# Optimization experiments

Hardware: AMD Instinct MI355X
Metric: run time of the kernel (lower is better)

The kernel has to match this reference:

```python
import jax, jax.numpy as jnp
import numpy as np

N_NODES = 50000
N_EDGES = 800000
IN_F, HID, OUT, FC_OUT = 192, 128, 64, 192


def setup_inputs() -> dict:
    key = jax.random.key(0)
    ks = jax.random.split(key, 12)
    s = 0.05
    return {
        "x": jax.random.normal(ks[0], (N_NODES, IN_F), dtype=jnp.float32),
        "edge_index": jax.random.randint(ks[1], (2, N_EDGES), 0, N_NODES, dtype=jnp.int64),
        "W1": jax.random.normal(ks[2], (IN_F, HID), dtype=jnp.float32) * s,
        "b1": jnp.zeros((HID,), jnp.float32),
        "Wg": jax.random.normal(ks[3], (HID, HID), dtype=jnp.float32) * s,
        "a_src": jax.random.normal(ks[4], (HID,), dtype=jnp.float32) * s,
        "a_dst": jax.random.normal(ks[5], (HID,), dtype=jnp.float32) * s,
        "bg": jnp.zeros((HID,), jnp.float32),
        "W2": jax.random.normal(ks[6], (HID, OUT), dtype=jnp.float32) * s,
        "b2": jnp.zeros((OUT,), jnp.float32),
        "Wf": jax.random.normal(ks[7], (OUT, FC_OUT), dtype=jnp.float32) * s,
        "bf": jnp.zeros((FC_OUT,), jnp.float32),
    }


def reference(x, edge_index, W1, b1, Wg, a_src, a_dst, bg, W2, b2, Wf, bf):
    N = x.shape[0]
    loops = jnp.arange(N, dtype=edge_index.dtype)
    src = jnp.concatenate([edge_index[0], loops])  # [E+N]
    dst = jnp.concatenate([edge_index[1], loops])

    # GCN symmetric normalization with self-loops (PyG gcn_norm)
    deg = jax.ops.segment_sum(jnp.ones_like(dst, dtype=x.dtype), dst, num_segments=N)
    dinv = jax.lax.rsqrt(jnp.maximum(deg, 1.0))  # deg >= 1 due to self-loops
    norm = dinv[src] * dinv[dst]  # [E+N]

    def gcn(h, W, b):
        h = h @ W
        out = jax.ops.segment_sum(h[src] * norm[:, None], dst, num_segments=N)
        return out + b

    h = gcn(x, W1, b1)  # [N, HID]

    # GAT layer (1 head, PyG defaults: self-loops, LeakyReLU(0.2), softmax over dst)
    hg = h @ Wg
    al = hg @ a_src  # [N]
    ar = hg @ a_dst  # [N]
    e = jax.nn.leaky_relu(al[src] + ar[dst], 0.2)  # [E+N]
    emax = jax.ops.segment_max(e, dst, num_segments=N)
    ex = jnp.exp(e - emax[dst])
    denom = jax.ops.segment_sum(ex, dst, num_segments=N)
    alpha = ex / denom[dst]
    h = jax.ops.segment_sum(hg[src] * alpha[:, None], dst, num_segments=N) + bg

    h = jax.nn.relu(h)
    h = gcn(h, W2, b2)  # [N, OUT]
    return h @ Wf + bf  # [N, 192]
```

## Files before the change

### kernel.cpp

```cpp
#include <hip/hip_runtime.h>
#include <hip/hip_fp16.h>
#include <cstdint>
#include <cstddef>

#define NN 50000
#define NE 800000
#define RNG 8
#define RSZ ((NN + RNG - 1) / RNG)
#define FIL_CPR 256
#define FILB (RNG*FIL_CPR)
#define CAP 64

typedef _Float16 half8 __attribute__((ext_vector_type(8)));
typedef float    f32x4 __attribute__((ext_vector_type(4)));

static __device__ __forceinline__ float lrelu02(float x){ return x > 0.f ? x : 0.2f*x; }

static __device__ __forceinline__ float2 h2f(uint32_t u){
  __half2 h = *reinterpret_cast<__half2*>(&u);
  return __half22float2(h);
}
static __device__ __forceinline__ uint32_t f2h(float a, float b){
  __half2 h = __floats2half2_rn(a, b);
  return *reinterpret_cast<uint32_t*>(&h);
}
static __device__ __forceinline__ void acc8p(float* acc, uint4 raw, float p){
  float2 f0=h2f(raw.x), f1=h2f(raw.y), f2=h2f(raw.z), f3=h2f(raw.w);
  acc[0]+=p*f0.x; acc[1]+=p*f0.y; acc[2]+=p*f1.x; acc[3]+=p*f1.y;
  acc[4]+=p*f2.x; acc[5]+=p*f2.y; acc[6]+=p*f3.x; acc[7]+=p*f3.y;
}
static __device__ __forceinline__ void acc8s(float* acc, uint4 raw){
  float2 f0=h2f(raw.x), f1=h2f(raw.y), f2=h2f(raw.z), f3=h2f(raw.w);
  acc[0]+=f0.x; acc[1]+=f0.y; acc[2]+=f1.x; acc[3]+=f1.y;
  acc[4]+=f2.x; acc[5]+=f2.y; acc[6]+=f3.x; acc[7]+=f3.y;
}

__global__ __launch_bounds__(256) void pack_all_kernel(
    const float* __restrict__ W1, const float* __restrict__ Wg,
    const float* __restrict__ W2, const float* __restrict__ Wf,
    _Float16* __restrict__ B1, _Float16* __restrict__ B2,
    _Float16* __restrict__ B3, _Float16* __restrict__ B4,
    int* __restrict__ fillp)
{
  const int b = blockIdx.x;
  if (b >= 240){
    const int i = (b - 240)*256 + threadIdx.x;
    if (i < NN) fillp[i] = 0;
    return;
  }
  const float* B; _Float16* O; int K, N, base;
  if      (b < 96)  { B = W1; O = B1; K = 192; N = 128; base = 0;   }
  else if (b < 160) { B = Wg; O = B2; K = 128; N = 128; base = 96;  }
  else if (b < 192) { B = W2; O = B3; K = 128; N = 64;  base = 160; }
  else              { B = Wf; O = B4; K = 64;  N = 192; base = 192; }
  const int i = (b - base)*256 + threadIdx.x;
  if (i >= K*N) return;
  const int j    = i & 7;
  const int lane = (i >> 3) & 63;
  const int tile = i >> 9;
  const int ntl  = N >> 4;
  const int ct   = tile % ntl;
  const int k0   = (tile / ntl) << 5;
  const int k = k0 + ((lane >> 4) << 3) + j;
  const int n = (ct << 4) + (lane & 15);
  O[i] = (_Float16)B[(size_t)k*N + n];
}

template<int K, int NT, bool AHALF, bool HALF_OUT, bool DOTS>
static __device__ __forceinline__ void gemm_block(
    const void* __restrict__ Av, const _Float16* __restrict__ Bsw,
    const float* __restrict__ bias, const float* __restrict__ rowscale,
    const float* __restrict__ avs, const float* __restrict__ avd,
    float* __restrict__ al, float* __restrict__ ar,
    void* __restrict__ Cv, int M, int N, int bm, int t)
{
  constexpr int NTL = NT*4;
  const int w    = t >> 6;
  const int lane = t & 63;
  const int m    = lane & 15;
  const int quad = lane >> 4;

  f32x4 acc[NTL];
  #pragma unroll
  for (int ct = 0; ct < NTL; ++ct) acc[ct] = (f32x4){0.f,0.f,0.f,0.f};

  const int row = bm + w*16 + m;
  const _Float16* bp = Bsw + lane*8;

  #pragma unroll
  for (int k0 = 0; k0 < K; k0 += 32){
    union { half8 h; uint4 u; uint32_t w[4]; } ua;
    if constexpr (AHALF){
      if (row < M){
        ua.u = *(const uint4*)((const _Float16*)Av + (size_t)row*K + k0 + quad*8);
      } else {
        ua.u = make_uint4(0u,0u,0u,0u);
      }
    } else {
      if (row < M){
        const float* Arow = (const float*)Av + (size_t)row*K;
        const float4 va = *(const float4*)(Arow + k0 + quad*8);
        const float4 vb = *(const float4*)(Arow + k0 + quad*8 + 4);
        ua.w[0] = f2h(va.x, va.y);
        ua.w[1] = f2h(va.z, va.w);
        ua.w[2] = f2h(vb.x, vb.y);
        ua.w[3] = f2h(vb.z, vb.w);
      } else {
        ua.u = make_uint4(0u,0u,0u,0u);
      }
    }
    const half8 af = ua.h;
    #pragma unroll
    for (int ct = 0; ct < NTL; ++ct){
      const half8 bf = *(const half8*)(bp + ((size_t)((k0>>5)*NTL + ct))*512);
      acc[ct] = __builtin_amdgcn_mfma_f32_16x16x32_f16(af, bf, acc[ct], 0, 0, 0);
    }
  }

  float rs[4];
  #pragma unroll
  for (int reg = 0; reg < 4; ++reg){
    const int r = bm + w*16 + quad*4 + reg;
    rs[reg] = (rowscale && r < M) ? rowscale[r] : 1.f;
  }
  float dal[4] = {0.f,0.f,0.f,0.f};
  float dar[4] = {0.f,0.f,0.f,0.f};
  #pragma unroll
  for (int ct = 0; ct < NTL; ++ct){
    const int colg = ct*16 + m;
    const float bv = bias ? bias[colg] : 0.f;
    float s_c = 0.f, d_c = 0.f;
    if constexpr (DOTS){ s_c = avs[colg]; d_c = avd[colg]; }
    #pragma unroll
    for (int reg = 0; reg < 4; ++reg){
      const int r = bm + w*16 + quad*4 + reg;
      if (r < M){
        const float v = rs[reg]*acc[ct][reg] + bv;
        if constexpr (DOTS){ dal[reg] += v*s_c; dar[reg] += v*d_c; }
        if constexpr (HALF_OUT){
          ((__half*)Cv)[(size_t)r*N + colg] = __float2half(v);
        } else {
          ((float*)Cv)[(size_t)r*N + colg] = v;
        }
      }
    }
  }
  if constexpr (DOTS){
    #pragma unroll
    for (int off = 1; off < 16; off <<= 1){
      #pragma unroll
      for (int reg = 0; reg < 4; ++reg){
        dal[reg] += __shfl_xor(dal[reg], off, 64);
        dar[reg] += __shfl_xor(dar[reg], off, 64);
      }
    }
    if (m == 0){
      #pragma unroll
      for (int reg = 0; reg < 4; ++reg){
        const int r = bm + w*16 + quad*4 + reg;
        if (r < M){
          al[r] = dal[reg];
          ar[r] = dar[reg];
        }
      }
    }
  }
}

template<int K, int NT, bool AHALF, bool HALF_OUT, bool DOTS>
__global__ __launch_bounds__(256) void gemm_mfma_kernel(
    const void* __restrict__ Av, const _Float16* __restrict__ Bsw,
    const float* __restrict__ bias, const float* __restrict__ rowscale,
    const float* __restrict__ avs, const float* __restrict__ avd,
    float* __restrict__ al, float* __restrict__ ar,
    void* __restrict__ Cv, int M, int N)
{
  gemm_block<K,NT,AHALF,HALF_OUT,DOTS>(Av, Bsw, bias, rowscale, avs, avd, al, ar,
                                       Cv, M, N, blockIdx.x*64, threadIdx.x);
}

__global__ __launch_bounds__(256) void gemm1_fill_kernel(
    const float* __restrict__ A, const _Float16* __restrict__ B1,
    __half* __restrict__ C, int M, int gm,
    const int* __restrict__ src, const int* __restrict__ dst,
    int* __restrict__ fillp, int* __restrict__ col, int E)
{
  if (blockIdx.x < (unsigned)gm){
    gemm_block<192,2,false,true,false>(A, B1, nullptr, nullptr, nullptr, nullptr,
                                       nullptr, nullptr, C, M, 128,
                                       blockIdx.x*64, threadIdx.x);
    return;
  }
  const int fb = blockIdx.x - gm;
  const int r  = fb % RNG;
  const int i  = fb / RNG;
  const int lo = r * RSZ;
  const int hi = min(lo + RSZ, NN);
  const int cs = (E + FIL_CPR - 1) / FIL_CPR;
  const int e1 = min((i+1)*cs, E);
  int e = i*cs + threadIdx.x;
  for (; e + 768 < e1; e += 1024){
    const int d0 = dst[e];       const int d1 = dst[e+256];
    const int d2 = dst[e+512];   const int d3 = dst[e+768];
    const int s0 = src[e];       const int s1 = src[e+256];
    const int s2 = src[e+512];   const int s3 = src[e+768];
    if (d0 >= lo && d0 < hi){ col[(d0<<6) + atomicAdd(&fillp[d0],1)] = s0; }
    if (d1 >= lo && d1 < hi){ col[(d1<<6) + atomicAdd(&fillp[d1],1)] = s1; }
    if (d2 >= lo && d2 < hi){ col[(d2<<6) + atomicAdd(&fillp[d2],1)] = s2; }
    if (d3 >= lo && d3 < hi){ col[(d3<<6) + atomicAdd(&fillp[d3],1)] = s3; }
  }
  for (; e < e1; e += 256){
    const int d = dst[e];
    if (d >= lo && d < hi){ col[(d<<6) + atomicAdd(&fillp[d],1)] = src[e]; }
  }
}

__global__ __launch_bounds__(256) void dinv_kernel(const int* __restrict__ len,
      float* __restrict__ dinv, int N){
  const int i = blockIdx.x*256 + threadIdx.x;
  if (i < N) dinv[i] = rsqrtf((float)(len[i] + 1));
}

__global__ __launch_bounds__(256) void gcn_agg128d_kernel(
    const __half* __restrict__ H, const int* __restrict__ len, const int* __restrict__ col,
    const float* __restrict__ dinv, const float* __restrict__ bias,
    __half* __restrict__ out, int N)
{
  const int t  = threadIdx.x;
  const int n  = blockIdx.x * 16 + (t >> 4);
  const int gl = t & 15;
  if (n >= N) return;
  const float dn = dinv[n];
  float acc[8];
  {
    uint4 raw = *(const uint4*)(H + (size_t)n*128 + gl*8);
    float2 f0=h2f(raw.x), f1=h2f(raw.y), f2=h2f(raw.z), f3=h2f(raw.w);
    acc[0]=dn*f0.x; acc[1]=dn*f0.y; acc[2]=dn*f1.x; acc[3]=dn*f1.y;
    acc[4]=dn*f2.x; acc[5]=dn*f2.y; acc[6]=dn*f3.x; acc[7]=dn*f3.y;
  }
  const int s0 = n << 6;
  const int s1 = s0 + len[n];
  for (int c0 = s0; c0 < s1; c0 += 16){
    const int nc = min(16, s1 - c0);
    int   sl = (gl < nc) ? col[c0 + gl] : 0;
    float dl = (gl < nc) ? dinv[sl] : 0.f;
    #pragma unroll 2
    for (int j = 0; j < nc; ++j){
      const int   s = __shfl(sl, j, 16);
      const float p = __shfl(dl, j, 16);
      acc8p(acc, *(const uint4*)(H + (size_t)s*128 + gl*8), p);
    }
  }
  const float* bp = bias + gl*8;
  float4 b0 = *(const float4*)(bp);
  float4 b1 = *(const float4*)(bp + 4);
  uint4 o;
  o.x = f2h(dn*acc[0] + b0.x, dn*acc[1] + b0.y);
  o.y = f2h(dn*acc[2] + b0.z, dn*acc[3] + b0.w);
  o.z = f2h(dn*acc[4] + b1.x, dn*acc[5] + b1.y);
  o.w = f2h(dn*acc[6] + b1.z, dn*acc[7] + b1.w);
  *(uint4*)(out + (size_t)n*128 + gl*8) = o;
}

__global__ __launch_bounds__(256) void gcn_agg64_kernel(
    const __half* __restrict__ H, const int* __restrict__ len, const int* __restrict__ col,
    const float* __restrict__ dinv, const float* __restrict__ bias,
    __half* __restrict__ out, int N)
{
  const int t  = threadIdx.x;
  const int n  = blockIdx.x * 32 + (t >> 3);
  const int gl = t & 7;
  if (n >= N) return;
  const float dn = dinv[n];
  float acc[8];
  {
    uint4 raw = *(const uint4*)(H + (size_t)n*64 + gl*8);
    float2 f0=h2f(raw.x), f1=h2f(raw.y), f2=h2f(raw.z), f3=h2f(raw.w);
    acc[0]=f0.x; acc[1]=f0.y; acc[2]=f1.x; acc[3]=f1.y;
    acc[4]=f2.x; acc[5]=f2.y; acc[6]=f3.x; acc[7]=f3.y;
  }
  const int s0 = n << 6;
  const int s1 = s0 + len[n];
  for (int c0 = s0; c0 < s1; c0 += 8){
    const int nc = min(8, s1 - c0);
    int sl = (gl < nc) ? col[c0 + gl] : 0;
    #pragma unroll 2
    for (int j = 0; j < nc; ++j){
      const int s = __shfl(sl, j, 8);
      acc8s(acc, *(const uint4*)(H + (size_t)s*64 + gl*8));
    }
  }
  const float* bp = bias + gl*8;
  float4 b0 = *(const float4*)(bp);
  float4 b1 = *(const float4*)(bp + 4);
  uint4 o;
  o.x = f2h(dn*acc[0] + b0.x, dn*acc[1] + b0.y);
  o.y = f2h(dn*acc[2] + b0.z, dn*acc[3] + b0.w);
  o.z = f2h(dn*acc[4] + b1.x, dn*acc[5] + b1.y);
  o.w = f2h(dn*acc[6] + b1.z, dn*acc[7] + b1.w);
  *(uint4*)(out + (size_t)n*64 + gl*8) = o;
}

__global__ __launch_bounds__(256) void gat_agg_kernel(
    const __half* __restrict__ HG, const int* __restrict__ len, const int* __restrict__ col,
    const float* __restrict__ al, const float* __restrict__ ar,
    const float* __restrict__ bias, __half* __restrict__ out, int N)
{
  const int t  = threadIdx.x;
  const int n  = blockIdx.x * 16 + (t >> 4);
  const int gl = t & 15;
  if (n >= N) return;
  const float arn = ar[n];
  const float pself = __expf(lrelu02(al[n] + arn));
  float lpart = 0.f;
  float acc[8];
  {
    uint4 raw = *(const uint4*)(HG + (size_t)n*128 + gl*8);
    float2 f0=h2f(raw.x), f1=h2f(raw.y), f2=h2f(raw.z), f3=h2f(raw.w);
    acc[0]=pself*f0.x; acc[1]=pself*f0.y; acc[2]=pself*f1.x; acc[3]=pself*f1.y;
    acc[4]=pself*f2.x; acc[5]=pself*f2.y; acc[6]=pself*f3.x; acc[7]=pself*f3.y;
  }
  const int s0 = n << 6;
  const int s1 = s0 + len[n];
  for (int c0 = s0; c0 < s1; c0 += 16){
    const int nc = min(16, s1 - c0);
    int   sl = (gl < nc) ? col[c0 + gl] : 0;
    float pl = (gl < nc) ? __expf(lrelu02(al[sl] + arn)) : 0.f;
    lpart += pl;
    #pragma unroll 2
    for (int j = 0; j < nc; ++j){
      const int   s = __shfl(sl, j, 16);
      const float p = __shfl(pl, j, 16);
      acc8p(acc, *(const uint4*)(HG + (size_t)s*128 + gl*8), p);
    }
  }
  #pragma unroll
  for (int off = 8; off > 0; off >>= 1) lpart += __shfl_xor(lpart, off, 16);
  const float inv = 1.f / (pself + lpart);
  const float* bp = bias + gl*8;
  float4 b0 = *(const float4*)(bp);
  float4 b1 = *(const float4*)(bp + 4);
  uint4 o;
  o.x = f2h(fmaxf(acc[0]*inv + b0.x, 0.f), fmaxf(acc[1]*inv + b0.y, 0.f));
  o.y = f2h(fmaxf(acc[2]*inv + b0.z, 0.f), fmaxf(acc[3]*inv + b0.w, 0.f));
  o.z = f2h(fmaxf(acc[4]*inv + b1.x, 0.f), fmaxf(acc[5]*inv + b1.y, 0.f));
  o.w = f2h(fmaxf(acc[6]*inv + b1.z, 0.f), fmaxf(acc[7]*inv + b1.w, 0.f));
  *(uint4*)(out + (size_t)n*128 + gl*8) = o;
}

extern "C" void kernel_launch(void* const* d_in, const int* in_sizes, int n_in,
                              void* d_out, int out_size, void* d_ws, size_t ws_size,
                              hipStream_t stream)
{
  const float* x     = (const float*)d_in[0];
  const int*   ei    = (const int*)d_in[1];
  const float* W1    = (const float*)d_in[2];
  const float* b1    = (const float*)d_in[3];
  const float* Wg    = (const float*)d_in[4];
  const float* a_src = (const float*)d_in[5];
  const float* a_dst = (const float*)d_in[6];
  const float* bg    = (const float*)d_in[7];
  const float* W2    = (const float*)d_in[8];
  const float* b2    = (const float*)d_in[9];
  const float* Wf    = (const float*)d_in[10];
  const float* bf    = (const float*)d_in[11];
  const int N = NN, E = NE;
  const int* src = ei;
  const int* dst = ei + E;

  char* p = (char*)d_ws;
  auto alloc = [&](size_t bytes)->char*{
    char* r = p; p += (bytes + 511) & ~size_t(511); return r;
  };
  int*      fillp = (int*)     alloc((size_t)N*4);
  int*      col   = (int*)     alloc((size_t)N*CAP*4);
  float*    dinv  = (float*)   alloc((size_t)N*4);
  float*    alar_ = (float*)   alloc((size_t)N*8);
  __half*   H16   = (__half*)  alloc((size_t)N*128*2);
  __half*   Hb    = (__half*)  alloc((size_t)N*128*2);
  _Float16* B1    = (_Float16*)alloc(24576*2);
  _Float16* B2    = (_Float16*)alloc(16384*2);
  _Float16* B3    = (_Float16*)alloc(8192*2);
  _Float16* B4    = (_Float16*)alloc(12288*2);
  float*    al    = alar_;
  float*    ar    = alar_ + N;

  const int gm  = (N + 63) / 64;
  const int g16 = (N + 15) / 16;
  const int g32 = (N + 31) / 32;

  pack_all_kernel<<<240 + (NN + 255)/256, 256, 0, stream>>>(
      W1, Wg, W2, Wf, B1, B2, B3, B4, fillp);

  gemm1_fill_kernel<<<gm + FILB, 256, 0, stream>>>(
      x, B1, H16, N, gm, src, dst, fillp, col, E);

  dinv_kernel<<<(N + 255)/256, 256, 0, stream>>>(fillp, dinv, N);

  gcn_agg128d_kernel<<<g16, 256, 0, stream>>>(H16, fillp, col, dinv, b1, Hb, N);
  gemm_mfma_kernel<128,2,true,true,true><<<gm, 256, 0, stream>>>(
      Hb, B2, nullptr, nullptr, a_src, a_dst, al, ar, H16, N, 128);
  gat_agg_kernel<<<g16, 256, 0, stream>>>(H16, fillp, col, al, ar, bg, Hb, N);
  gemm_mfma_kernel<128,1,true,true,false><<<gm, 256, 0, stream>>>(
      Hb, B3, nullptr, dinv, nullptr, nullptr, nullptr, nullptr, H16, N, 64);
  gcn_agg64_kernel<<<g32, 256, 0, stream>>>(H16, fillp, col, dinv, b2, Hb, N);
  gemm_mfma_kernel<64,3,true,false,false><<<gm, 256, 0, stream>>>(
      Hb, B4, bf, nullptr, nullptr, nullptr, nullptr, nullptr, d_out, N, 192);
}
```

Before: 276.7 us.

## Fold Wg into W1 by associativity and fuse attention dots into first aggregation

```diff
diff --git a/kernel.cpp b/kernel.cpp
--- a/kernel.cpp
+++ b/kernel.cpp
@@ -38,21 +38,30 @@
 __global__ __launch_bounds__(256) void pack_all_kernel(
     const float* __restrict__ W1, const float* __restrict__ Wg,
     const float* __restrict__ W2, const float* __restrict__ Wf,
-    _Float16* __restrict__ B1, _Float16* __restrict__ B2,
-    _Float16* __restrict__ B3, _Float16* __restrict__ B4,
-    int* __restrict__ fillp)
+    const float* __restrict__ b1,
+    _Float16* __restrict__ B1, _Float16* __restrict__ B3, _Float16* __restrict__ B4,
+    float* __restrict__ bg1, int* __restrict__ fillp)
 {
   const int b = blockIdx.x;
-  if (b >= 240){
-    const int i = (b - 240)*256 + threadIdx.x;
-    if (i < NN) fillp[i] = 0;
+  if (b >= 176){
+    if (b < 372){
+      const int i = (b - 176)*256 + threadIdx.x;
+      if (i < NN) fillp[i] = 0;
+    } else {
+      const int n = threadIdx.x;
+      if (n < 128){
+        float s = 0.f;
+        #pragma unroll 4
+        for (int c = 0; c < 128; ++c) s += b1[c]*Wg[c*128 + n];
+        bg1[n] = s;
+      }
+    }
     return;
   }
-  const float* B; _Float16* O; int K, N, base;
-  if      (b < 96)  { B = W1; O = B1; K = 192; N = 128; base = 0;   }
-  else if (b < 160) { B = Wg; O = B2; K = 128; N = 128; base = 96;  }
-  else if (b < 192) { B = W2; O = B3; K = 128; N = 64;  base = 160; }
-  else              { B = Wf; O = B4; K = 64;  N = 192; base = 192; }
+  const float* B; _Float16* O; int K, N, base; bool fused = false;
+  if      (b < 96)  { B = W1; O = B1; K = 192; N = 128; base = 0;  fused = true; }
+  else if (b < 128) { B = W2; O = B3; K = 128; N = 64;  base = 96;  }
+  else              { B = Wf; O = B4; K = 64;  N = 192; base = 128; }
   const int i = (b - base)*256 + threadIdx.x;
   if (i >= K*N) return;
   const int j    = i & 7;
@@ -63,15 +72,20 @@
   const int k0   = (tile / ntl) << 5;
   const int k = k0 + ((lane >> 4) << 3) + j;
   const int n = (ct << 4) + (lane & 15);
-  O[i] = (_Float16)B[(size_t)k*N + n];
-}
-
-template<int K, int NT, bool AHALF, bool HALF_OUT, bool DOTS>
+  if (fused){
+    float s = 0.f;
+    #pragma unroll 4
+    for (int c = 0; c < 128; ++c) s += W1[k*128 + c]*Wg[c*128 + n];
+    O[i] = (_Float16)s;
+  } else {
+    O[i] = (_Float16)B[(size_t)k*N + n];
+  }
+}
+
+template<int K, int NT, bool AHALF, bool HALF_OUT, bool RSLEN>
 static __device__ __forceinline__ void gemm_block(
     const void* __restrict__ Av, const _Float16* __restrict__ Bsw,
-    const float* __restrict__ bias, const float* __restrict__ rowscale,
-    const float* __restrict__ avs, const float* __restrict__ avd,
-    float* __restrict__ al, float* __restrict__ ar,
+    const float* __restrict__ bias, const int* __restrict__ rslen,
     void* __restrict__ Cv, int M, int N, int bm, int t)
 {
   constexpr int NTL = NT*4;
@@ -121,22 +135,18 @@
   #pragma unroll
   for (int reg = 0; reg < 4; ++reg){
     const int r = bm + w*16 + quad*4 + reg;
-    rs[reg] = (rowscale && r < M) ? rowscale[r] : 1.f;
-  }
-  float dal[4] = {0.f,0.f,0.f,0.f};
-  float dar[4] = {0.f,0.f,0.f,0.f};
+    rs[reg] = 1.f;
+    if constexpr (RSLEN){ if (r < M) rs[reg] = rsqrtf((float)(rslen[r] + 1)); }
+  }
   #pragma unroll
   for (int ct = 0; ct < NTL; ++ct){
     const int colg = ct*16 + m;
     const float bv = bias ? bias[colg] : 0.f;
-    float s_c = 0.f, d_c = 0.f;
-    if constexpr (DOTS){ s_c = avs[colg]; d_c = avd[colg]; }
     #pragma unroll
     for (int reg = 0; reg < 4; ++reg){
       const int r = bm + w*16 + quad*4 + reg;
       if (r < M){
         const float v = rs[reg]*acc[ct][reg] + bv;
-        if constexpr (DOTS){ dal[reg] += v*s_c; dar[reg] += v*d_c; }
         if constexpr (HALF_OUT){
           ((__half*)Cv)[(size_t)r*N + colg] = __float2half(v);
         } else {
@@ -145,38 +155,16 @@
       }
     }
   }
-  if constexpr (DOTS){
-    #pragma unroll
-    for (int off = 1; off < 16; off <<= 1){
-      #pragma unroll
-      for (int reg = 0; reg < 4; ++reg){
-        dal[reg] += __shfl_xor(dal[reg], off, 64);
-        dar[reg] += __shfl_xor(dar[reg], off, 64);
-      }
-    }
-    if (m == 0){
-      #pragma unroll
-      for (int reg = 0; reg < 4; ++reg){
-        const int r = bm + w*16 + quad*4 + reg;
-        if (r < M){
-          al[r] = dal[reg];
-          ar[r] = dar[reg];
-        }
-      }
-    }
-  }
-}
-
-template<int K, int NT, bool AHALF, bool HALF_OUT, bool DOTS>
+}
+
+template<int K, int NT, bool AHALF, bool HALF_OUT, bool RSLEN>
 __global__ __launch_bounds__(256) void gemm_mfma_kernel(
     const void* __restrict__ Av, const _Float16* __restrict__ Bsw,
-    const float* __restrict__ bias, const float* __restrict__ rowscale,
-    const float* __restrict__ avs, const float* __restrict__ avd,
-    float* __restrict__ al, float* __restrict__ ar,
+    const float* __restrict__ bias, const int* __restrict__ rslen,
     void* __restrict__ Cv, int M, int N)
 {
-  gemm_block<K,NT,AHALF,HALF_OUT,DOTS>(Av, Bsw, bias, rowscale, avs, avd, al, ar,
-                                       Cv, M, N, blockIdx.x*64, threadIdx.x);
+  gemm_block<K,NT,AHALF,HALF_OUT,RSLEN>(Av, Bsw, bias, rslen, Cv, M, N,
+                                        blockIdx.x*64, threadIdx.x);
 }
 
 __global__ __launch_bounds__(256) void gemm1_fill_kernel(
@@ -186,8 +174,7 @@
     int* __restrict__ fillp, int* __restrict__ col, int E)
 {
   if (blockIdx.x < (unsigned)gm){
-    gemm_block<192,2,false,true,false>(A, B1, nullptr, nullptr, nullptr, nullptr,
-                                       nullptr, nullptr, C, M, 128,
+    gemm_block<192,2,false,true,false>(A, B1, nullptr, nullptr, C, M, 128,
                                        blockIdx.x*64, threadIdx.x);
     return;
   }
@@ -215,90 +202,57 @@
   }
 }
 
-__global__ __launch_bounds__(256) void dinv_kernel(const int* __restrict__ len,
-      float* __restrict__ dinv, int N){
-  const int i = blockIdx.x*256 + threadIdx.x;
-  if (i < N) dinv[i] = rsqrtf((float)(len[i] + 1));
-}
-
-__global__ __launch_bounds__(256) void gcn_agg128d_kernel(
-    const __half* __restrict__ H, const int* __restrict__ len, const int* __restrict__ col,
-    const float* __restrict__ dinv, const float* __restrict__ bias,
-    __half* __restrict__ out, int N)
+__global__ __launch_bounds__(256) void agg1_kernel(
+    const __half* __restrict__ T, const int* __restrict__ len, const int* __restrict__ col,
+    const float* __restrict__ bg1, const float* __restrict__ avs,
+    const float* __restrict__ avd,
+    __half* __restrict__ hg, float* __restrict__ al, float* __restrict__ ar, int N)
 {
   const int t  = threadIdx.x;
   const int n  = blockIdx.x * 16 + (t >> 4);
   const int gl = t & 15;
   if (n >= N) return;
-  const float dn = dinv[n];
+  const int ln = len[n];
+  const float dn = rsqrtf((float)(ln + 1));
   float acc[8];
   {
-    uint4 raw = *(const uint4*)(H + (size_t)n*128 + gl*8);
+    uint4 raw = *(const uint4*)(T + (size_t)n*128 + gl*8);
     float2 f0=h2f(raw.x), f1=h2f(raw.y), f2=h2f(raw.z), f3=h2f(raw.w);
     acc[0]=dn*f0.x; acc[1]=dn*f0.y; acc[2]=dn*f1.x; acc[3]=dn*f1.y;
     acc[4]=dn*f2.x; acc[5]=dn*f2.y; acc[6]=dn*f3.x; acc[7]=dn*f3.y;
   }
   const int s0 = n << 6;
-  const int s1 = s0 + len[n];
+  const int s1 = s0 + ln;
   for (int c0 = s0; c0 < s1; c0 += 16){
     const int nc = min(16, s1 - c0);
     int   sl = (gl < nc) ? col[c0 + gl] : 0;
-    float dl = (gl < nc) ? dinv[sl] : 0.f;
-    #pragma unroll 2
+    float dl = (gl < nc) ? rsqrtf((float)(len[sl] + 1)) : 0.f;
+    #pragma unroll 4
     for (int j = 0; j < nc; ++j){
       const int   s = __shfl(sl, j, 16);
       const float p = __shfl(dl, j, 16);
-      acc8p(acc, *(const uint4*)(H + (size_t)s*128 + gl*8), p);
-    }
-  }
-  const float* bp = bias + gl*8;
-  float4 b0 = *(const float4*)(bp);
-  float4 b1 = *(const float4*)(bp + 4);
+      acc8p(acc, *(const uint4*)(T + (size_t)s*128 + gl*8), p);
+    }
+  }
+  const float* bp = bg1 + gl*8;
+  float v[8];
+  #pragma unroll
+  for (int i = 0; i < 8; ++i) v[i] = dn*acc[i] + bp[i];
   uint4 o;
-  o.x = f2h(dn*acc[0] + b0.x, dn*acc[1] + b0.y);
-  o.y = f2h(dn*acc[2] + b0.z, dn*acc[3] + b0.w);
-  o.z = f2h(dn*acc[4] + b1.x, dn*acc[5] + b1.y);
-  o.w = f2h(dn*acc[6] + b1.z, dn*acc[7] + b1.w);
-  *(uint4*)(out + (size_t)n*128 + gl*8) = o;
-}
-
-__global__ __launch_bounds__(256) void gcn_agg64_kernel(
-    const __half* __restrict__ H, const int* __restrict__ len, const int* __restrict__ col,
-    const float* __restrict__ dinv, const float* __restrict__ bias,
-    __half* __restrict__ out, int N)
-{
-  const int t  = threadIdx.x;
-  const int n  = blockIdx.x * 32 + (t >> 3);
-  const int gl = t & 7;
-  if (n >= N) return;
-  const float dn = dinv[n];
-  float acc[8];
-  {
-    uint4 raw = *(const uint4*)(H + (size_t)n*64 + gl*8);
-    float2 f0=h2f(raw.x), f1=h2f(raw.y), f2=h2f(raw.z), f3=h2f(raw.w);
-    acc[0]=f0.x; acc[1]=f0.y; acc[2]=f1.x; acc[3]=f1.y;
-    acc[4]=f2.x; acc[5]=f2.y; acc[6]=f3.x; acc[7]=f3.y;
-  }
-  const int s0 = n << 6;
-  const int s1 = s0 + len[n];
-  for (int c0 = s0; c0 < s1; c0 += 8){
-    const int nc = min(8, s1 - c0);
-    int sl = (gl < nc) ? col[c0 + gl] : 0;
-    #pragma unroll 2
-    for (int j = 0; j < nc; ++j){
-      const int s = __shfl(sl, j, 8);
-      acc8s(acc, *(const uint4*)(H + (size_t)s*64 + gl*8));
-    }
-  }
-  const float* bp = bias + gl*8;
-  float4 b0 = *(const float4*)(bp);
-  float4 b1 = *(const float4*)(bp + 4);
-  uint4 o;
-  o.x = f2h(dn*acc[0] + b0.x, dn*acc[1] + b0.y);
-  o.y = f2h(dn*acc[2] + b0.z, dn*acc[3] + b0.w);
-  o.z = f2h(dn*acc[4] + b1.x, dn*acc[5] + b1.y);
-  o.w = f2h(dn*acc[6] + b1.z, dn*acc[7] + b1.w);
-  *(uint4*)(out + (size_t)n*64 + gl*8) = o;
+  o.x = f2h(v[0], v[1]); o.y = f2h(v[2], v[3]);
+  o.z = f2h(v[4], v[5]); o.w = f2h(v[6], v[7]);
+  *(uint4*)(hg + (size_t)n*128 + gl*8) = o;
+  const float* asp = avs + gl*8;
+  const float* adp = avd + gl*8;
+  float sal = 0.f, sar = 0.f;
+  #pragma unroll
+  for (int i = 0; i < 8; ++i){ sal += v[i]*asp[i]; sar += v[i]*adp[i]; }
+  #pragma unroll
+  for (int off = 8; off > 0; off >>= 1){
+    sal += __shfl_xor(sal, off, 16);
+    sar += __shfl_xor(sar, off, 16);
+  }
+  if (gl == 0){ al[n] = sal; ar[n] = sar; }
 }
 
 __global__ __launch_bounds__(256) void gat_agg_kernel(
@@ -327,7 +281,7 @@
     int   sl = (gl < nc) ? col[c0 + gl] : 0;
     float pl = (gl < nc) ? __expf(lrelu02(al[sl] + arn)) : 0.f;
     lpart += pl;
-    #pragma unroll 2
+    #pragma unroll 4
     for (int j = 0; j < nc; ++j){
       const int   s = __shfl(sl, j, 16);
       const float p = __shfl(pl, j, 16);
@@ -346,6 +300,45 @@
   o.z = f2h(fmaxf(acc[4]*inv + b1.x, 0.f), fmaxf(acc[5]*inv + b1.y, 0.f));
   o.w = f2h(fmaxf(acc[6]*inv + b1.z, 0.f), fmaxf(acc[7]*inv + b1.w, 0.f));
   *(uint4*)(out + (size_t)n*128 + gl*8) = o;
+}
+
+__global__ __launch_bounds__(256) void gcn_agg64_kernel(
+    const __half* __restrict__ H, const int* __restrict__ len, const int* __restrict__ col,
+    const float* __restrict__ bias, __half* __restrict__ out, int N)
+{
+  const int t  = threadIdx.x;
+  const int n  = blockIdx.x * 32 + (t >> 3);
+  const int gl = t & 7;
+  if (n >= N) return;
+  const int ln = len[n];
+  const float dn = rsqrtf((float)(ln + 1));
+  float acc[8];
+  {
+    uint4 raw = *(const uint4*)(H + (size_t)n*64 + gl*8);
+    float2 f0=h2f(raw.x), f1=h2f(raw.y), f2=h2f(raw.z), f3=h2f(raw.w);
+    acc[0]=f0.x; acc[1]=f0.y; acc[2]=f1.x; acc[3]=f1.y;
+    acc[4]=f2.x; acc[5]=f2.y; acc[6]=f3.x; acc[7]=f3.y;
+  }
+  const int s0 = n << 6;
+  const int s1 = s0 + ln;
+  for (int c0 = s0; c0 < s1; c0 += 8){
+    const int nc = min(8, s1 - c0);
+    int sl = (gl < nc) ? col[c0 + gl] : 0;
+    #pragma unroll 4
+    for (int j = 0; j < nc; ++j){
+      const int s = __shfl(sl, j, 8);
+      acc8s(acc, *(const uint4*)(H + (size_t)s*64 + gl*8));
+    }
+  }
+  const float* bp = bias + gl*8;
+  float4 b0 = *(const float4*)(bp);
+  float4 b1 = *(const float4*)(bp + 4);
+  uint4 o;
+  o.x = f2h(dn*acc[0] + b0.x, dn*acc[1] + b0.y);
+  o.y = f2h(dn*acc[2] + b0.z, dn*acc[3] + b0.w);
+  o.z = f2h(dn*acc[4] + b1.x, dn*acc[5] + b1.y);
+  o.w = f2h(dn*acc[6] + b1.z, dn*acc[7] + b1.w);
+  *(uint4*)(out + (size_t)n*64 + gl*8) = o;
 }
 
 extern "C" void kernel_launch(void* const* d_in, const int* in_sizes, int n_in,
@@ -374,14 +367,13 @@
   };
   int*      fillp = (int*)     alloc((size_t)N*4);
   int*      col   = (int*)     alloc((size_t)N*CAP*4);
-  float*    dinv  = (float*)   alloc((size_t)N*4);
   float*    alar_ = (float*)   alloc((size_t)N*8);
-  __half*   H16   = (__half*)  alloc((size_t)N*128*2);
-  __half*   Hb    = (__half*)  alloc((size_t)N*128*2);
+  __half*   HA    = (__half*)  alloc((size_t)N*128*2);
+  __half*   HB    = (__half*)  alloc((size_t)N*128*2);
   _Float16* B1    = (_Float16*)alloc(24576*2);
-  _Float16* B2    = (_Float16*)alloc(16384*2);
   _Float16* B3    = (_Float16*)alloc(8192*2);
   _Float16* B4    = (_Float16*)alloc(12288*2);
+  float*    bg1   = (float*)   alloc(128*4);
   float*    al    = alar_;
   float*    ar    = alar_ + N;
 
@@ -389,21 +381,18 @@
   const int g16 = (N + 15) / 16;
   const int g32 = (N + 31) / 32;
 
-  pack_all_kernel<<<240 + (NN + 255)/256, 256, 0, stream>>>(
-      W1, Wg, W2, Wf, B1, B2, B3, B4, fillp);
+  pack_all_kernel<<<373, 256, 0, stream>>>(
+      W1, Wg, W2, Wf, b1, B1, B3, B4, bg1, fillp);
 
   gemm1_fill_kernel<<<gm + FILB, 256, 0, stream>>>(
-      x, B1, H16, N, gm, src, dst, fillp, col, E);
-
-  dinv_kernel<<<(N + 255)/256, 256, 0, stream>>>(fillp, dinv, N);
-
-  gcn_agg128d_kernel<<<g16, 256, 0, stream>>>(H16, fillp, col, dinv, b1, Hb, N);
-  gemm_mfma_kernel<128,2,true,true,true><<<gm, 256, 0, stream>>>(
-      Hb, B2, nullptr, nullptr, a_src, a_dst, al, ar, H16, N, 128);
-  gat_agg_kernel<<<g16, 256, 0, stream>>>(H16, fillp, col, al, ar, bg, Hb, N);
-  gemm_mfma_kernel<128,1,true,true,false><<<gm, 256, 0, stream>>>(
-      Hb, B3, nullptr, dinv, nullptr, nullptr, nullptr, nullptr, H16, N, 64);
-  gcn_agg64_kernel<<<g32, 256, 0, stream>>>(H16, fillp, col, dinv, b2, Hb, N);
+      x, B1, HA, N, gm, src, dst, fillp, col, E);
+
+  agg1_kernel<<<g16, 256, 0, stream>>>(HA, fillp, col, bg1, a_src, a_dst,
+                                       HB, al, ar, N);
+  gat_agg_kernel<<<g16, 256, 0, stream>>>(HB, fillp, col, al, ar, bg, HA, N);
+  gemm_mfma_kernel<128,1,true,true,true><<<gm, 256, 0, stream>>>(
+      HA, B3, nullptr, fillp, HB, N, 64);
+  gcn_agg64_kernel<<<g32, 256, 0, stream>>>(HB, fillp, col, b2, HA, N);
   gemm_mfma_kernel<64,3,true,false,false><<<gm, 256, 0, stream>>>(
-      Hb, B4, bf, nullptr, nullptr, nullptr, nullptr, nullptr, d_out, N, 192);
-}
+      HA, B4, bf, nullptr, d_out, N, 192);
+}
```

After: 264.0 us. 1.05x faster.
